# Optimization experiments

Measured on AMD Instinct MI355X. Metric: run time of the kernel, lower is better.

## Reference

```python
import jax, jax.numpy as jnp
import numpy as np

C = 5.0          # tanh clamp constant (args.c, non-trainable)
B, N, R, D = 4, 16, 64, 256  # batch, block_num, block_len, word_dim
NEG = -1e9


def setup_inputs() -> dict:
    key = jax.random.key(0)
    ks = iter(jax.random.split(key, 80))

    def W(i, o):
        # xavier-like init (torch stores (out,in); we store (in,out) and use x @ W)
        return jax.random.normal(next(ks), (i, o), jnp.float32) * np.float32(np.sqrt(2.0 / (i + o)))

    def bvec(d):
        return jax.random.normal(next(ks), (d,), jnp.float32) * 0.01

    inp = {"x": jax.random.normal(next(ks), (B, N, R, D), jnp.float32)}
    for p in ("fw", "bw"):
        inp[f"fcW_{p}"] = W(D, D);  inp[f"fcb_{p}"] = bvec(D)
        inp[f"mW1_{p}"] = W(D, D);  inp[f"mW2_{p}"] = W(D, D);  inp[f"mb_{p}"] = bvec(D)
        inp[f"s2tW1_{p}"] = W(D, D); inp[f"s2tb1_{p}"] = bvec(D)
        inp[f"s2tW_{p}"] = W(D, D);  inp[f"s2tb_{p}"] = bvec(D)
        inp[f"gW1_{p}"] = W(D, D);  inp[f"gW2_{p}"] = W(D, D);  inp[f"gb_{p}"] = bvec(D)
        inp[f"fW1_{p}"] = W(3 * D, D); inp[f"fb1_{p}"] = bvec(D)
        inp[f"fW2_{p}"] = W(3 * D, D); inp[f"fb2_{p}"] = bvec(D)
    return inp


def _mSA(x, W1, W2, b, fw):
    # x: (..., L, d) -> (..., L, d). Additive per-feature attention with strict
    # triangular mask. fw: token i attends to j > i (last row zeroed);
    # bw: token i attends to j < i (first row zeroed). Matches the torch
    # -inf mask + narrow + zero-pad construction exactly.
    L = x.shape[-2]
    xi = (x @ W1)[..., :, None, :]                 # (..., L, 1, d)
    xj = (x @ W2)[..., None, :, :]                 # (..., 1, L, d)
    f = C * jnp.tanh((xi + xj + b) / C)            # (..., i, j, d)
    i = jnp.arange(L)[:, None]
    j = jnp.arange(L)[None, :]
    allowed = (j > i) if fw else (j < i)           # (L, L)
    scores = jnp.where(allowed[..., None], f, NEG)
    att = jax.nn.softmax(scores, axis=-2)          # softmax over j
    rowvalid = (jnp.arange(L) < L - 1) if fw else (jnp.arange(L) > 0)
    att = att * rowvalid[:, None, None].astype(x.dtype)
    return jnp.einsum('...ijd,...jd->...id', att, x)


def _s2t(x, W1, b1, Wo, bo):
    # source2token self-attention: (..., L, d) -> (..., d)
    f = jax.nn.relu(x @ W1 + b1)
    a = jax.nn.softmax(f @ Wo + bo, axis=-2)
    return jnp.sum(a * x, axis=-2)


def _mblosa(x, mW1, mW2, mb, s2tW1, s2tb1, s2tW, s2tb,
            gW1, gW2, gb, fW1, fb1, fW2, fb2, fw):
    Bb, n, r, d = x.shape
    h = _mSA(x, mW1, mW2, mb, fw)                  # (B, n, r, d) intra-block
    v = _s2t(h, s2tW1, s2tb1, s2tW, s2tb)          # (B, n, d)    block summary
    o = _mSA(v, mW1, mW2, mb, fw)                  # (B, n, d)    inter-block
    G = jax.nn.sigmoid(o @ gW1 + v @ gW2 + gb)
    e = G * o + (1.0 - G) * v                      # (B, n, d)
    # torch: cat of e[i] repeated r times, then narrow(1, 0, n)
    idx = jnp.arange(n) // r
    E = e[:, idx]                                  # (B, n, d)
    # torch: flatten blocks then narrow(1, 0, n) (faithful to source)
    xf = x.reshape(Bb, n * r, d)[:, :n]
    hf = h.reshape(Bb, n * r, d)[:, :n]
    cat = jnp.concatenate([xf, hf, E], axis=-1)    # (B, n, 3d)
    fusion = jax.nn.relu(cat @ fW1 + fb1)
    Gf = jax.nn.sigmoid(cat @ fW2 + fb2)
    return Gf * fusion + (1.0 - Gf) * xf           # (B, n, d)


def reference(x,
              fcW_fw, fcb_fw, mW1_fw, mW2_fw, mb_fw, s2tW1_fw, s2tb1_fw,
              s2tW_fw, s2tb_fw, gW1_fw, gW2_fw, gb_fw, fW1_fw, fb1_fw,
              fW2_fw, fb2_fw,
              fcW_bw, fcb_bw, mW1_bw, mW2_bw, mb_bw, s2tW1_bw, s2tb1_bw,
              s2tW_bw, s2tb_bw, gW1_bw, gW2_bw, gb_bw, fW1_bw, fb1_bw,
              fW2_bw, fb2_bw):
    in_fw = jax.nn.relu(x @ fcW_fw + fcb_fw)
    in_bw = jax.nn.relu(x @ fcW_bw + fcb_bw)
    u_fw = _mblosa(in_fw, mW1_fw, mW2_fw, mb_fw, s2tW1_fw, s2tb1_fw,
                   s2tW_fw, s2tb_fw, gW1_fw, gW2_fw, gb_fw,
                   fW1_fw, fb1_fw, fW2_fw, fb2_fw, True)
    u_bw = _mblosa(in_bw, mW1_bw, mW2_bw, mb_bw, s2tW1_bw, s2tb1_bw,
                   s2tW_bw, s2tb_bw, gW1_bw, gW2_bw, gb_bw,
                   fW1_bw, fb1_bw, fW2_bw, fb2_bw, False)
    return jnp.concatenate([u_fw, u_bw], axis=-1)  # (B, n, 2d)
```

## Files before the change

### kernel.cpp

```cpp
#include <hip/hip_runtime.h>
#include <hip/hip_bf16.h>

typedef __hip_bfloat16 BF16;
typedef __attribute__((ext_vector_type(8))) short short8;
typedef __attribute__((ext_vector_type(4))) short short4v;
typedef __attribute__((ext_vector_type(4))) float f32x4;
typedef __attribute__((ext_vector_type(2))) float f32x2;

#define MFMA_B16(a,b,c) __builtin_amdgcn_mfma_f32_16x16x32_bf16((a),(b),(c),0,0,0)

__device__ __forceinline__ short f2bs(float f){ BF16 h = __float2bfloat16(f); return *(short*)&h; }
__device__ __forceinline__ float bs2f(short s){ BF16 h = *(BF16*)&s; return __bfloat162float(h); }

struct SrcPack { const float* s[10]; };

__global__ __launch_bounds__(256) void prep_k(SrcPack p, const float* __restrict__ xsrc,
    short* __restrict__ Oh, short* __restrict__ Ol,
    short* __restrict__ xH, short* __restrict__ xL)
{
    if (blockIdx.y < 10) {
        __shared__ float s[64][65];
        const float* W = p.s[blockIdx.y];
        short* oh = Oh + (size_t)blockIdx.y * 65536;
        short* ol = Ol + (size_t)blockIdx.y * 65536;
        int tr = (blockIdx.x >> 2) * 64, tc = (blockIdx.x & 3) * 64;
        #pragma unroll
        for (int i = 0; i < 16; i++) {
            int e = threadIdx.x + i * 256;
            int r = e >> 6, c = e & 63;
            s[c][r] = W[(size_t)(tr + r) * 256 + tc + c];
        }
        __syncthreads();
        #pragma unroll
        for (int i = 0; i < 16; i++) {
            int e = threadIdx.x + i * 256;
            int c2 = e >> 6, r2 = e & 63;
            float v = s[c2][r2];
            short hi = f2bs(v);
            short lo = f2bs(v - bs2f(hi));
            size_t oi = (size_t)(tc + c2) * 256 + tr + r2;
            oh[oi] = hi;
            ol[oi] = lo;
        }
    } else {
        size_t base0 = (size_t)(blockIdx.y - 10) * 524288
                     + (size_t)blockIdx.x * 32768 + threadIdx.x * 4;
        for (int it = 0; it < 32; it++) {
            size_t idx = base0 + (size_t)it * 1024;
            float4 f = *(const float4*)&xsrc[idx];
            float v[4] = {f.x, f.y, f.z, f.w};
            short4v h, lo;
            #pragma unroll
            for (int t = 0; t < 4; t++) {
                h[t] = f2bs(v[t]);
                lo[t] = f2bs(v[t] - bs2f(h[t]));
            }
            *(short4v*)&xH[idx] = h;
            *(short4v*)&xL[idx] = lo;
        }
    }
}

template<int AM, int OM, int RELU, int BS>
__device__ __forceinline__ void gemm_body(const void* __restrict__ A0,
    const void* __restrict__ Alo,
    const short* __restrict__ Wh, const short* __restrict__ Wl,
    const float* __restrict__ bias, void* __restrict__ O0, void* __restrict__ O1,
    int row0, int col0)
{
    constexpr int LDK = 72;
    __shared__ short sAh[64 * LDK];
    __shared__ short sAl[(AM == 0) ? 8 : 64 * LDK];
    __shared__ short sBh[64 * LDK];
    __shared__ short sBl[BS ? 8 : 64 * LDK];
    int tid = threadIdx.x;
    int w = tid >> 6, l = tid & 63;
    int m = l & 15, q = l >> 4;
    int sr = w * 16 + m;

    f32x4 acc[4];
    #pragma unroll
    for (int cf = 0; cf < 4; cf++) acc[cf] = (f32x4)(0.f);

    for (int kh = 0; kh < 4; kh++) {
        int kbase = kh * 64;
        #pragma unroll
        for (int i = 0; i < 2; i++) {
            int kl = q * 8 + 32 * i;
            size_t gofs = (size_t)(row0 + sr) * 256 + kbase + kl;
            if (AM == 1) {
                const float* src = (const float*)A0 + gofs;
                float4 f0 = *(const float4*)src;
                float4 f1 = *(const float4*)(src + 4);
                short8 vh, vl;
                float tmp[8] = {f0.x, f0.y, f0.z, f0.w, f1.x, f1.y, f1.z, f1.w};
                #pragma unroll
                for (int j = 0; j < 8; j++) {
                    vh[j] = f2bs(tmp[j]);
                    vl[j] = f2bs(tmp[j] - bs2f(vh[j]));
                }
                *(short8*)&sAh[sr * LDK + kl] = vh;
                *(short8*)&sAl[sr * LDK + kl] = vl;
            } else if (AM == 2) {
                *(short8*)&sAh[sr * LDK + kl] = *(const short8*)((const short*)A0 + gofs);
                *(short8*)&sAl[sr * LDK + kl] = *(const short8*)((const short*)Alo + gofs);
            } else {
                *(short8*)&sAh[sr * LDK + kl] = *(const short8*)((const short*)A0 + gofs);
            }
            size_t gofsB = (size_t)(col0 + sr) * 256 + kbase + kl;
            *(short8*)&sBh[sr * LDK + kl] = *(const short8*)(Wh + gofsB);
            if (!BS)
                *(short8*)&sBl[sr * LDK + kl] = *(const short8*)(Wl + gofsB);
        }
        __syncthreads();
        #pragma unroll
        for (int ch = 0; ch < 2; ch++) {
            int k = ch * 32 + q * 8;
            short8 ah = *(const short8*)&sAh[(w * 16 + m) * LDK + k];
            short8 al = (AM != 0) ? *(const short8*)&sAl[(w * 16 + m) * LDK + k] : ah;
            #pragma unroll
            for (int cf = 0; cf < 4; cf++) {
                short8 bh = *(const short8*)&sBh[(cf * 16 + m) * LDK + k];
                acc[cf] = MFMA_B16(ah, bh, acc[cf]);
                if (!BS) {
                    short8 bl = *(const short8*)&sBl[(cf * 16 + m) * LDK + k];
                    acc[cf] = MFMA_B16(ah, bl, acc[cf]);
                }
                if (AM != 0)
                    acc[cf] = MFMA_B16(al, bh, acc[cf]);
            }
        }
        __syncthreads();
    }
    #pragma unroll
    for (int cf = 0; cf < 4; cf++) {
        int col = col0 + cf * 16 + m;
        float bv = bias ? bias[col] : 0.f;
        #pragma unroll
        for (int r = 0; r < 4; r++) {
            int row = row0 + w * 16 + q * 4 + r;
            float v = acc[cf][r] + bv;
            if (RELU) v = fmaxf(v, 0.f);
            size_t oi = (size_t)row * 256 + col;
            if (OM == 0) {
                ((float*)O0)[oi] = v;
            } else if (OM == 1) {
                ((short*)O0)[oi] = f2bs(v);
            } else {
                short hi = f2bs(v);
                ((short*)O0)[oi] = hi;
                ((short*)O1)[oi] = f2bs(v - bs2f(hi));
            }
        }
    }
}

struct GDir { const void* A0; const void* Al; const short* Wh; const short* Wl;
              const float* bias; void* O0; void* O1; };

template<int AM, int OM, int RELU, int BS>
__global__ __launch_bounds__(256) void gemm_k(GDir p0, GDir p1)
{
    GDir p = blockIdx.z ? p1 : p0;
    gemm_body<AM, OM, RELU, BS>(p.A0, p.Al, p.Wh, p.Wl, p.bias, p.O0, p.O1,
                                blockIdx.x * 64, blockIdx.y * 64);
}

struct G2Dir { const float* A; const short* W1h; const short* W1l;
               const short* W2h; const short* W2l; const float* b2;
               float* C1; float* C2; };

__global__ __launch_bounds__(256) void gemm2s_k(G2Dir p0, G2Dir p1)
{
    G2Dir p = blockIdx.z ? p1 : p0;
    int y = blockIdx.y;
    const short* Wh = (y < 4) ? p.W1h : p.W2h;
    const short* Wl = (y < 4) ? p.W1l : p.W2l;
    void* C = (y < 4) ? (void*)p.C1 : (void*)p.C2;
    const float* bias = (y < 4) ? nullptr : p.b2;
    gemm_body<1, 0, 0, 0>(p.A, nullptr, Wh, Wl, bias, C, nullptr, 0, (y & 3) * 64);
}

struct MbloDir { const short* Ah; const short* Al;
                 const short* W1h; const short* W2h;
                 const float* mb; short* Hh; short* Hl; int fw; };

__global__ __launch_bounds__(512) void mblo_k(MbloDir p0, MbloDir p1)
{
    __shared__ char smraw[50688] __attribute__((aligned(16)));
    short* gAh  = (short*)smraw;
    short* gAl  = gAh + 4608;
    short* gB1h = gAh + 9216;
    short* gB2h = gAh + 13824;
    float* aP  = (float*)smraw;
    float* aQt = aP + 4224;
    float* aXt = aP + 8448;

    MbloDir p = blockIdx.z ? p1 : p0;
    int tid = threadIdx.x;
    int w = tid >> 6, l = tid & 63;
    int m = l & 15, q = l >> 4;
    int rh = w >> 1;
    int cb = (w & 1) * 2;
    int row0 = blockIdx.x * 64, d0 = blockIdx.y * 64;
    int srow = tid >> 3;
    int skl  = (tid & 7) * 8;

    f32x4 acc1[2], acc2[2];
    #pragma unroll
    for (int cf = 0; cf < 2; cf++) { acc1[cf] = (f32x4)(0.f); acc2[cf] = (f32x4)(0.f); }

    for (int kh = 0; kh < 4; kh++) {
        int kbase = kh * 64;
        size_t ga = (size_t)(row0 + srow) * 256 + kbase + skl;
        *(short8*)&gAh[srow * 72 + skl] = *(const short8*)(p.Ah + ga);
        *(short8*)&gAl[srow * 72 + skl] = *(const short8*)(p.Al + ga);
        size_t gb = (size_t)(d0 + srow) * 256 + kbase + skl;
        *(short8*)&gB1h[srow * 72 + skl] = *(const short8*)(p.W1h + gb);
        *(short8*)&gB2h[srow * 72 + skl] = *(const short8*)(p.W2h + gb);
        __syncthreads();
        #pragma unroll
        for (int ch = 0; ch < 2; ch++) {
            int k = ch * 32 + q * 8;
            short8 ah = *(const short8*)&gAh[(rh * 16 + m) * 72 + k];
            short8 al = *(const short8*)&gAl[(rh * 16 + m) * 72 + k];
            #pragma unroll
            for (int cf = 0; cf < 2; cf++) {
                int bofs = ((cb + cf) * 16 + m) * 72 + k;
                short8 b1 = *(const short8*)&gB1h[bofs];
                acc1[cf] = MFMA_B16(ah, b1, acc1[cf]);
                acc1[cf] = MFMA_B16(al, b1, acc1[cf]);
                short8 b2 = *(const short8*)&gB2h[bofs];
                acc2[cf] = MFMA_B16(ah, b2, acc2[cf]);
                acc2[cf] = MFMA_B16(al, b2, acc2[cf]);
            }
        }
        __syncthreads();
    }
    #pragma unroll
    for (int cf = 0; cf < 2; cf++) {
        int col = (cb + cf) * 16 + m;
        float mbv = p.mb[d0 + col];
        #pragma unroll
        for (int r = 0; r < 4; r++) {
            int row = rh * 16 + q * 4 + r;
            aP[row * 66 + col]  = __expf(0.4f * acc1[cf][r]);
            aQt[col * 66 + row] = __expf(0.4f * (acc2[cf][r] + mbv));
        }
    }
    {
        size_t gx = (size_t)(row0 + srow) * 256 + d0 + skl;
        short8 xh = *(const short8*)(p.Ah + gx);
        short8 xl = *(const short8*)(p.Al + gx);
        #pragma unroll
        for (int t = 0; t < 8; t++)
            aXt[(skl + t) * 66 + srow] = bs2f(xh[t]) + bs2f(xl[t]);
    }
    __syncthreads();
    float Pr[8], den[8], num[8];
    #pragma unroll
    for (int t8 = 0; t8 < 8; t8++) {
        Pr[t8] = aP[(w + 8 * t8) * 66 + l];
        den[t8] = 0.f; num[t8] = 0.f;
    }
    for (int jc = 0; jc < 4; jc++) {
        f32x2 qv[8], xv[8];
        #pragma unroll
        for (int u = 0; u < 8; u++) {
            qv[u] = *(const f32x2*)&aQt[l * 66 + jc * 16 + u * 2];
            xv[u] = *(const f32x2*)&aXt[l * 66 + jc * 16 + u * 2];
        }
        #pragma unroll
        for (int t8 = 0; t8 < 8; t8++) {
            int i = w + 8 * t8;
            if (p.fw) { if (jc * 16 + 15 <= i) continue; }
            else      { if (jc * 16 >= i) continue; }
            float P = Pr[t8];
            float d_ = den[t8], n_ = num[t8];
            #pragma unroll
            for (int u = 0; u < 8; u++)
            #pragma unroll
            for (int v2 = 0; v2 < 2; v2++) {
                int j = jc * 16 + u * 2 + v2;
                float uu = P * qv[u][v2];
                float r = __builtin_amdgcn_rcpf(1.f + uu);
                float wgt = __expf(-10.f * r);
                bool ok = p.fw ? (j > i) : (j < i);
                wgt = ok ? wgt : 0.f;
                d_ += wgt;
                n_ += wgt * xv[u][v2];
            }
            den[t8] = d_; num[t8] = n_;
        }
    }
    #pragma unroll
    for (int t8 = 0; t8 < 8; t8++) {
        int i = w + 8 * t8;
        bool valid = p.fw ? (i < 63) : (i > 0);
        float out = valid ? (num[t8] * __builtin_amdgcn_rcpf(den[t8])) : 0.f;
        short hi = f2bs(out);
        size_t oi = (size_t)(row0 + i) * 256 + d0 + l;
        p.Hh[oi] = hi;
        p.Hl[oi] = f2bs(out - bs2f(hi));
    }
}

struct PoolDir { const short* T1; const short* Wh; const float* bias;
                 const short* Hh; const short* Hl; float* V; };

__global__ __launch_bounds__(256) void s2t_pool_k(PoolDir p0, PoolDir p1)
{
    __shared__ char smraw[37888] __attribute__((aligned(16)));
    short* gAh = (short*)smraw;
    short* gBh = gAh + 4608;
    float* aL = (float*)smraw;
    float* aH = aL + 4352;
    float* rm = aL + 8704;
    float* rd = aL + 8960;
    float* rn = aL + 9216;

    PoolDir p = blockIdx.z ? p1 : p0;
    int tid = threadIdx.x;
    int w = tid >> 6, l = tid & 63;
    int m = l & 15, q = l >> 4;
    int sr = w * 16 + m;
    int row0 = blockIdx.x * 64, d0 = blockIdx.y * 64;

    f32x4 acc[4];
    #pragma unroll
    for (int cf = 0; cf < 4; cf++) acc[cf] = (f32x4)(0.f);

    for (int kh = 0; kh < 4; kh++) {
        int kbase = kh * 64;
        #pragma unroll
        for (int i = 0; i < 2; i++) {
            int kl = q * 8 + 32 * i;
            *(short8*)&gAh[sr * 72 + kl] =
                *(const short8*)(p.T1 + (size_t)(row0 + sr) * 256 + kbase + kl);
            *(short8*)&gBh[sr * 72 + kl] =
                *(const short8*)(p.Wh + (size_t)(d0 + sr) * 256 + kbase + kl);
        }
        __syncthreads();
        #pragma unroll
        for (int ch = 0; ch < 2; ch++) {
            int k = ch * 32 + q * 8;
            short8 ah = *(const short8*)&gAh[(w * 16 + m) * 72 + k];
            #pragma unroll
            for (int cf = 0; cf < 4; cf++) {
                short8 bh = *(const short8*)&gBh[(cf * 16 + m) * 72 + k];
                acc[cf] = MFMA_B16(ah, bh, acc[cf]);
            }
        }
        __syncthreads();
    }
    #pragma unroll
    for (int cf = 0; cf < 4; cf++) {
        int col = cf * 16 + m;
        float bv = p.bias[d0 + col];
        #pragma unroll
        for (int r = 0; r < 4; r++) {
            int row = w * 16 + q * 4 + r;
            aL[row * 68 + col] = acc[cf][r] + bv;
        }
    }
    #pragma unroll
    for (int it = 0; it < 2; it++) {
        int e = tid + it * 256;
        int j = e >> 3, d8 = (e & 7) * 8;
        short8 xh = *(const short8*)(p.Hh + (size_t)(row0 + j) * 256 + d0 + d8);
        short8 xl = *(const short8*)(p.Hl + (size_t)(row0 + j) * 256 + d0 + d8);
        #pragma unroll
        for (int t = 0; t < 8; t++)
            aH[j * 68 + d8 + t] = bs2f(xh[t]) + bs2f(xl[t]);
    }
    __syncthreads();
    int dl = tid & 63, rq = tid >> 6;
    float mx = -1e30f, den = 0.f, num = 0.f;
    #pragma unroll
    for (int rr = 0; rr < 16; rr++) {
        int r = rq * 16 + rr;
        float lv = aL[r * 68 + dl];
        float hv = aH[r * 68 + dl];
        if (lv > mx) {
            float sc = __expf(mx - lv);
            den *= sc; num *= sc; mx = lv;
        }
        float wgt = __expf(lv - mx);
        den += wgt; num += wgt * hv;
    }
    rm[rq * 64 + dl] = mx; rd[rq * 64 + dl] = den; rn[rq * 64 + dl] = num;
    __syncthreads();
    if (rq == 0) {
        float M = fmaxf(fmaxf(rm[dl], rm[64 + dl]), fmaxf(rm[128 + dl], rm[192 + dl]));
        float D = 0.f, Nn = 0.f;
        #pragma unroll
        for (int k = 0; k < 4; k++) {
            float sc = __expf(rm[k * 64 + dl] - M);
            D += rd[k * 64 + dl] * sc;
            Nn += rn[k * 64 + dl] * sc;
        }
        p.V[(size_t)blockIdx.x * 256 + d0 + dl] = Nn / D;
    }
}

struct GateDir { const float* vW1; const float* vW2; const float* V;
                 const float* gW1; const float* gW2; const float* gb;
                 float* E0; int fw; };

__global__ __launch_bounds__(256) void attn2gate_k(GateDir p0, GateDir p1)
{
    GateDir p = blockIdx.z ? p1 : p0;
    __shared__ float so[256], sv[256], red[4][64];
    int b = blockIdx.x, k = threadIdx.x;
    float o = 0.f;
    if (p.fw) {
        float qv = p.vW1[(size_t)(b * 16) * 256 + k];
        float den = 0.f, num = 0.f;
        for (int j = 1; j < 16; j++) {
            float z = (qv + p.vW2[(size_t)(b * 16 + j) * 256 + k]) * 0.2f;
            float e2 = __expf(2.f * z);
            float t = 1.f - 2.f / (e2 + 1.f);
            float wgt = __expf(5.f * t);
            den += wgt; num += wgt * p.V[(size_t)(b * 16 + j) * 256 + k];
        }
        o = num / den;
    }
    so[k] = o;
    sv[k] = p.V[(size_t)(b * 16) * 256 + k];
    __syncthreads();
    int c = k & 63, ks = k >> 6;
    int gc = blockIdx.y * 64 + c;
    float acc = 0.f;
    int k0 = ks * 64;
    #pragma unroll 8
    for (int kk = 0; kk < 64; kk++) {
        int kx = k0 + kk;
        acc += so[kx] * p.gW1[(size_t)kx * 256 + gc] + sv[kx] * p.gW2[(size_t)kx * 256 + gc];
    }
    red[ks][c] = acc;
    __syncthreads();
    if (ks == 0) {
        float a = red[0][c] + red[1][c] + red[2][c] + red[3][c] + p.gb[gc];
        float G = 1.f / (1.f + __expf(-a));
        p.E0[b * 256 + gc] = G * so[gc] + (1.f - G) * sv[gc];
    }
}

struct FuseDir { const short* INh; const short* INl; const short* Hh; const short* Hl;
                 const float* E0; const float* fW1; const float* fb1;
                 const float* fW2; const float* fb2; };

__global__ __launch_bounds__(256) void fusion_k(FuseDir p0, FuseDir p1, float* __restrict__ out)
{
    FuseDir p = blockIdx.z ? p1 : p0;
    __shared__ float cat[768];
    __shared__ float red1[4][64], red2[4][64];
    int bt = blockIdx.x, b = bt >> 4, t = bt & 15;
    int c = threadIdx.x & 63, ks = threadIdx.x >> 6;
    int gc = blockIdx.y * 64 + c;
    size_t xrow = ((size_t)b * 1024 + t) * 256;
    cat[threadIdx.x]       = bs2f(p.INh[xrow + threadIdx.x]) + bs2f(p.INl[xrow + threadIdx.x]);
    cat[256 + threadIdx.x] = bs2f(p.Hh[xrow + threadIdx.x]) + bs2f(p.Hl[xrow + threadIdx.x]);
    cat[512 + threadIdx.x] = p.E0[b * 256 + threadIdx.x];
    __syncthreads();
    float a1 = 0.f, a2 = 0.f;
    int k0 = ks * 192;
    #pragma unroll 8
    for (int kk = 0; kk < 192; kk++) {
        int k = k0 + kk;
        float cv = cat[k];
        a1 += cv * p.fW1[(size_t)k * 256 + gc];
        a2 += cv * p.fW2[(size_t)k * 256 + gc];
    }
    red1[ks][c] = a1; red2[ks][c] = a2;
    __syncthreads();
    if (ks == 0) {
        float s1 = red1[0][c] + red1[1][c] + red1[2][c] + red1[3][c] + p.fb1[gc];
        float s2 = red2[0][c] + red2[1][c] + red2[2][c] + red2[3][c] + p.fb2[gc];
        float fus = fmaxf(s1, 0.f);
        float Gf = 1.f / (1.f + __expf(-s2));
        float u = Gf * fus + (1.f - Gf) * cat[gc];
        out[((size_t)(b * 16 + t)) * 512 + (size_t)blockIdx.z * 256 + gc] = u;
    }
}

extern "C" void kernel_launch(void* const* d_in, const int* in_sizes, int n_in,
                              void* d_out, int out_size, void* d_ws, size_t ws_size,
                              hipStream_t stream)
{
    const float* x = (const float*)d_in[0];
    char* base = (char*)d_ws;
    auto alloc = [&](size_t bytes){ void* r = base; base += (bytes + 255) & ~255ULL; return r; };
    short* inH = (short*)alloc(2 * 1048576 * 2);
    short* inL = (short*)alloc(2 * 1048576 * 2);
    short* hH  = (short*)alloc(2 * 1048576 * 2);
    short* hL  = (short*)alloc(2 * 1048576 * 2);
    short* t1  = (short*)alloc(2 * 1048576 * 2);
    short* xH  = (short*)alloc(1048576 * 2);
    short* xL  = (short*)alloc(1048576 * 2);
    short* wtH = (short*)alloc(10 * 65536 * 2);
    short* wtL = (short*)alloc(10 * 65536 * 2);
    float* v   = (float*)alloc(2 * 16384 * 4);
    float* vW1 = (float*)alloc(2 * 16384 * 4);
    float* vW2 = (float*)alloc(2 * 16384 * 4);
    float* E0  = (float*)alloc(2 * 1024 * 4);

    SrcPack sp;
    const int src_idx[5] = {0, 2, 3, 5, 7};
    for (int p = 0; p < 2; p++)
        for (int i = 0; i < 5; i++)
            sp.s[p * 5 + i] = (const float*)d_in[1 + p * 16 + src_idx[i]];
    prep_k<<<dim3(16, 12), 256, 0, stream>>>(sp, x, wtH, wtL, xH, xL);

    GDir fc[2], s2t1[2];
    MbloDir mbd[2];
    PoolDir pld[2];
    G2Dir g2d[2];
    GateDir gtd[2];
    FuseDir fsd[2];
    for (int p = 0; p < 2; p++) {
        int bi = 1 + p * 16;
        const float* fcb   = (const float*)d_in[bi + 1];
        const float* mb    = (const float*)d_in[bi + 4];
        const float* s2tb1 = (const float*)d_in[bi + 6];
        const float* s2tb  = (const float*)d_in[bi + 8];
        size_t po = (size_t)p * 1048576;
        const short* W0h = wtH + (size_t)(p * 5 + 0) * 65536, *W0l = wtL + (size_t)(p * 5 + 0) * 65536;
        const short* W1h = wtH + (size_t)(p * 5 + 1) * 65536, *W1l = wtL + (size_t)(p * 5 + 1) * 65536;
        const short* W2h = wtH + (size_t)(p * 5 + 2) * 65536, *W2l = wtL + (size_t)(p * 5 + 2) * 65536;
        const short* W3h = wtH + (size_t)(p * 5 + 3) * 65536;
        const short* W4h = wtH + (size_t)(p * 5 + 4) * 65536;

        fc[p]   = { xH, xL, W0h, W0l, fcb, inH + po, inL + po };
        mbd[p]  = { inH + po, inL + po, W1h, W2h, mb, hH + po, hL + po, (p == 0) };
        s2t1[p] = { hH + po, hL + po, W3h, nullptr, s2tb1, t1 + po, nullptr };
        pld[p]  = { t1 + po, W4h, s2tb, hH + po, hL + po, v + p * 16384 };
        g2d[p]  = { v + p * 16384, W1h, W1l, W2h, W2l, mb, vW1 + p * 16384, vW2 + p * 16384 };
        gtd[p]  = { vW1 + p * 16384, vW2 + p * 16384, v + p * 16384,
                    (const float*)d_in[bi + 9], (const float*)d_in[bi + 10],
                    (const float*)d_in[bi + 11], E0 + p * 1024, (p == 0) };
        fsd[p]  = { inH + po, inL + po, hH + po, hL + po, E0 + p * 1024,
                    (const float*)d_in[bi + 12], (const float*)d_in[bi + 13],
                    (const float*)d_in[bi + 14], (const float*)d_in[bi + 15] };
    }

    gemm_k<2, 2, 1, 0><<<dim3(64, 4, 2), 256, 0, stream>>>(fc[0], fc[1]);
    mblo_k<<<dim3(64, 4, 2), 512, 0, stream>>>(mbd[0], mbd[1]);
    gemm_k<2, 1, 1, 1><<<dim3(64, 4, 2), 256, 0, stream>>>(s2t1[0], s2t1[1]);
    s2t_pool_k<<<dim3(64, 4, 2), 256, 0, stream>>>(pld[0], pld[1]);
    gemm2s_k<<<dim3(1, 8, 2), 256, 0, stream>>>(g2d[0], g2d[1]);
    attn2gate_k<<<dim3(4, 4, 2), 256, 0, stream>>>(gtd[0], gtd[1]);
    fusion_k<<<dim3(64, 4, 2), 256, 0, stream>>>(fsd[0], fsd[1], (float*)d_out);
}
```

Before: 223.1 us.

## Restructure masked attention inner loop with exact bounds, folded exp2 constants, interleaved Q/X

The per-feature attention loop in mblo_k now iterates only over the valid j range for each row instead of 16-wide chunks with per-element masking. It folds the -10 and ln2 scaling into P so each weight costs one fma, one rcp and one native exp2. Q and X are interleaved in a single LDS array so each (q, x) pair comes from one 8-byte load. The risks are load imbalance between waves, because triangular trip counts differ per row, and the loss of the register-cached Q/X reuse across rows.

```diff
diff --git a/kernel.cpp b/kernel.cpp
--- a/kernel.cpp
+++ b/kernel.cpp
@@ -8,6 +8,12 @@
 typedef __attribute__((ext_vector_type(2))) float f32x2;
 
 #define MFMA_B16(a,b,c) __builtin_amdgcn_mfma_f32_16x16x32_bf16((a),(b),(c),0,0,0)
+
+#if __has_builtin(__builtin_amdgcn_exp2f)
+#define EXP2F(x) __builtin_amdgcn_exp2f(x)
+#else
+#define EXP2F(x) __expf(0.6931471805599453f * (x))
+#endif
 
 __device__ __forceinline__ short f2bs(float f){ BF16 h = __float2bfloat16(f); return *(short*)&h; }
 __device__ __forceinline__ float bs2f(short s){ BF16 h = *(BF16*)&s; return __bfloat162float(h); }
@@ -187,14 +193,15 @@
 
 __global__ __launch_bounds__(512) void mblo_k(MbloDir p0, MbloDir p1)
 {
-    __shared__ char smraw[50688] __attribute__((aligned(16)));
+    __shared__ char smraw[50176] __attribute__((aligned(16)));
     short* gAh  = (short*)smraw;
     short* gAl  = gAh + 4608;
     short* gB1h = gAh + 9216;
     short* gB2h = gAh + 13824;
     float* aP  = (float*)smraw;
-    float* aQt = aP + 4224;
-    float* aXt = aP + 8448;
+    float* aQX = aP + 4224;
+
+    const float KLN = -0.06931471805599453f;
 
     MbloDir p = blockIdx.z ? p1 : p0;
     int tid = threadIdx.x;
@@ -244,8 +251,8 @@
         #pragma unroll
         for (int r = 0; r < 4; r++) {
             int row = rh * 16 + q * 4 + r;
-            aP[row * 66 + col]  = __expf(0.4f * acc1[cf][r]);
-            aQt[col * 66 + row] = __expf(0.4f * (acc2[cf][r] + mbv));
+            aP[row * 66 + col] = __expf(0.4f * acc1[cf][r]) * KLN;
+            aQX[col * 130 + 2 * row] = __expf(0.4f * (acc2[cf][r] + mbv));
         }
     }
     {
@@ -254,50 +261,40 @@
         short8 xl = *(const short8*)(p.Al + gx);
         #pragma unroll
         for (int t = 0; t < 8; t++)
-            aXt[(skl + t) * 66 + srow] = bs2f(xh[t]) + bs2f(xl[t]);
-    }
-    __syncthreads();
-    float Pr[8], den[8], num[8];
-    #pragma unroll
-    for (int t8 = 0; t8 < 8; t8++) {
-        Pr[t8] = aP[(w + 8 * t8) * 66 + l];
-        den[t8] = 0.f; num[t8] = 0.f;
-    }
-    for (int jc = 0; jc < 4; jc++) {
-        f32x2 qv[8], xv[8];
-        #pragma unroll
-        for (int u = 0; u < 8; u++) {
-            qv[u] = *(const f32x2*)&aQt[l * 66 + jc * 16 + u * 2];
-            xv[u] = *(const f32x2*)&aXt[l * 66 + jc * 16 + u * 2];
-        }
-        #pragma unroll
-        for (int t8 = 0; t8 < 8; t8++) {
-            int i = w + 8 * t8;
-            if (p.fw) { if (jc * 16 + 15 <= i) continue; }
-            else      { if (jc * 16 >= i) continue; }
-            float P = Pr[t8];
-            float d_ = den[t8], n_ = num[t8];
-            #pragma unroll
-            for (int u = 0; u < 8; u++)
-            #pragma unroll
-            for (int v2 = 0; v2 < 2; v2++) {
-                int j = jc * 16 + u * 2 + v2;
-                float uu = P * qv[u][v2];
-                float r = __builtin_amdgcn_rcpf(1.f + uu);
-                float wgt = __expf(-10.f * r);
-                bool ok = p.fw ? (j > i) : (j < i);
-                wgt = ok ? wgt : 0.f;
-                d_ += wgt;
-                n_ += wgt * xv[u][v2];
-            }
-            den[t8] = d_; num[t8] = n_;
-        }
-    }
+            aQX[(skl + t) * 130 + 2 * srow + 1] = bs2f(xh[t]) + bs2f(xl[t]);
+    }
+    __syncthreads();
+    const float* lane_qx = &aQX[l * 130];
     #pragma unroll
     for (int t8 = 0; t8 < 8; t8++) {
         int i = w + 8 * t8;
+        float Pp = aP[i * 66 + l];
+        int js = p.fw ? (i + 1) : 0;
+        int je = p.fw ? 64 : i;
+        float den0 = 0.f, den1 = 0.f, num0 = 0.f, num1 = 0.f;
+        int j = js;
+        for (; j + 4 <= je; j += 4) {
+            f32x2 qx0 = *(const f32x2*)&lane_qx[2 * j];
+            f32x2 qx1 = *(const f32x2*)&lane_qx[2 * j + 2];
+            f32x2 qx2 = *(const f32x2*)&lane_qx[2 * j + 4];
+            f32x2 qx3 = *(const f32x2*)&lane_qx[2 * j + 6];
+            float w0 = EXP2F(__builtin_amdgcn_rcpf(fmaf(Pp, qx0[0], KLN)));
+            float w1 = EXP2F(__builtin_amdgcn_rcpf(fmaf(Pp, qx1[0], KLN)));
+            float w2 = EXP2F(__builtin_amdgcn_rcpf(fmaf(Pp, qx2[0], KLN)));
+            float w3 = EXP2F(__builtin_amdgcn_rcpf(fmaf(Pp, qx3[0], KLN)));
+            den0 += w0; num0 = fmaf(w0, qx0[1], num0);
+            den1 += w1; num1 = fmaf(w1, qx1[1], num1);
+            den0 += w2; num0 = fmaf(w2, qx2[1], num0);
+            den1 += w3; num1 = fmaf(w3, qx3[1], num1);
+        }
+        for (; j < je; j++) {
+            f32x2 qx = *(const f32x2*)&lane_qx[2 * j];
+            float wgt = EXP2F(__builtin_amdgcn_rcpf(fmaf(Pp, qx[0], KLN)));
+            den0 += wgt; num0 = fmaf(wgt, qx[1], num0);
+        }
+        float den = den0 + den1, num = num0 + num1;
         bool valid = p.fw ? (i < 63) : (i > 0);
-        float out = valid ? (num[t8] * __builtin_amdgcn_rcpf(den[t8])) : 0.f;
+        float out = valid ? (num * __builtin_amdgcn_rcpf(den)) : 0.f;
         short hi = f2bs(out);
         size_t oi = (size_t)(row0 + i) * 256 + d0 + l;
         p.Hh[oi] = hi;
```

Result: faster. 210.8 us (-5.5%).
